# Optimization experiments

Hardware: AMD Instinct MI355X
Metric: run time of the kernel (lower is better)

The kernel has to match this reference:

```python
import jax, jax.numpy as jnp
import numpy as np

M_HIST = 5        # Anderson history depth (m=5 in anderson_solver)
N_POWER = 20      # power iterations to estimate sigma for spectral_norm
REG = 1e-4        # Tikhonov regularization on the Anderson LS system
MAX_ITER = 25     # deq_max_iter


def _l2norm(x):
    return x / (jnp.linalg.norm(x) + 1e-12)


def spectral_normalize(W):
    # torch spectral_norm: W / sigma, sigma = u^T W v with u,v from power iteration
    u = _l2norm(jnp.ones((W.shape[0],), W.dtype))
    def body(_, u):
        v = _l2norm(W.T @ u)
        return _l2norm(W @ v)
    u = jax.lax.fori_loop(0, N_POWER, body, u)
    v = _l2norm(W.T @ u)
    u = jax.lax.stop_gradient(u)
    v = jax.lax.stop_gradient(v)
    sigma = u @ (W @ v)
    return W / sigma


def make_f(W1, b1, W2, b2):
    W1s = spectral_normalize(W1)
    W2s = spectral_normalize(W2)
    def f(z, context):
        h = jnp.tanh(jnp.concatenate([z, context], axis=-1) @ W1s.T + b1)
        return jnp.tanh(h @ W2s.T + b2)
    return f


def anderson(f, x0, context, max_iter, m=M_HIST):
    # Mirrors anderson_solver, including its duplicated warm-up step.
    X = [x0]
    F = [f(x0, context)]
    x = F[0]; X.append(x); F.append(f(x, context))
    x = F[0]; X.append(x); F.append(f(x, context))
    for _k in range(2, max_iter):
        m_k = min(len(X) - 1, m)
        dX = jnp.stack([X[-i] - X[-i - 1] for i in range(1, m_k + 1)], axis=-1)  # [B,d,mk]
        dF = jnp.stack([F[-i] - F[-i - 1] for i in range(1, m_k + 1)], axis=-1)
        dG = dF - dX
        A = jnp.einsum('bdi,bdj->bij', dG, dG) + REG * jnp.eye(m_k, dtype=x0.dtype)
        r = F[-1] - X[-1]
        Bv = jnp.einsum('bdi,bd->bi', dG, r)
        alpha = jnp.linalg.solve(A, Bv[..., None])[..., 0]          # [B,mk]
        x = F[-1] - jnp.einsum('bdi,bi->bd', dF, alpha)
        X.append(x)
        F.append(f(x, context))
        if len(X) > m + 1:
            X.pop(0); F.pop(0)
    return X[-1]


def setup_inputs() -> dict:
    key = jax.random.key(0)
    ks = jax.random.split(key, 5)
    B, X_DIM, LATENT, HIDDEN = 2048, 256, 256, 1024
    context = jax.random.normal(ks[0], (B, X_DIM), jnp.float32)
    W1 = jax.random.normal(ks[1], (HIDDEN, LATENT + X_DIM), jnp.float32) / np.sqrt(LATENT + X_DIM)
    b1 = jax.random.normal(ks[2], (HIDDEN,), jnp.float32) * 0.01
    W2 = jax.random.normal(ks[3], (LATENT, HIDDEN), jnp.float32) / np.sqrt(HIDDEN)
    b2 = jax.random.normal(ks[4], (LATENT,), jnp.float32) * 0.01
    return {"context": context, "W1": W1, "b1": b1, "W2": W2, "b2": b2}


def reference(context, W1, b1, W2, b2):
    f = make_f(W1, b1, W2, b2)
    z0 = jnp.zeros((context.shape[0], W2.shape[0]), context.dtype)
    z_star = anderson(f, z0, context, MAX_ITER)
    return z_star
```

## Files before the change

### kernel.cpp

```cpp
#include <hip/hip_runtime.h>
#include <hip/hip_bf16.h>


#define B_ROWS 2048
#define D_LAT  256
#define D_CTX  256
#define D_HID  1024
#define KCAT   512
#define SLOT   (B_ROWS * D_LAT)
#define NRING  7

typedef __bf16 bf16x8 __attribute__((ext_vector_type(8)));
typedef float f32x4 __attribute__((ext_vector_type(4)));
typedef unsigned short u16;

__global__ void init_kernel(const float* __restrict__ ctx,
                            __hip_bfloat16* __restrict__ zc,
                            float* __restrict__ vA, float* __restrict__ uA,
                            float* __restrict__ G1p, float* __restrict__ G2) {
  int i = blockIdx.x * 256 + threadIdx.x;
  if (i < B_ROWS * KCAT) {
    int b = i >> 9, c = i & 511;
    float v = (c < 256) ? 0.0f : ctx[b * 256 + (c - 256)];
    zc[i] = __float2bfloat16(v);
  }
  if (i < 512 * 512) G1p[i] = 0.0f;
  if (i < 256 * 256) G2[i] = 0.0f;
  if (i < KCAT) vA[i] = 0.0f;
  if (i < D_LAT) uA[i] = 1.0f;
}

__global__ __launch_bounds__(256) void gram_kernel(
    const float* __restrict__ W1, const float* __restrict__ W2,
    float* __restrict__ G1p, float* __restrict__ G2) {
  __shared__ float As[32][66];
  __shared__ float Bs[32][34];
  const int tid = threadIdx.x;
  const int tx = tid & 15, ty = tid >> 4;

  const float* X; float* G; int N, ti, tj, k0base; bool modeA;
  int b = blockIdx.x;
  if (b < 1024) {
    modeA = true; X = W1; G = G1p; N = 512;
    int s = b >> 7, t = b & 127;
    ti = t >> 4; tj = t & 15; k0base = s * 128;
  } else {
    modeA = false; b -= 1024; X = W2; G = G2; N = 256;
    int s = b >> 5, t = b & 31;
    ti = t >> 3; tj = t & 7; k0base = s * 128;
  }

  float acc[4][2] = {};
  for (int k0 = k0base; k0 < k0base + 128; k0 += 32) {
    if (modeA) {
      for (int idx = tid; idx < 2048; idx += 256) {
        int r = idx & 63, c = idx >> 6;
        As[c][r] = X[(size_t)(k0 + c) * 512 + ti * 64 + r];
      }
      for (int idx = tid; idx < 1024; idx += 256) {
        int r = idx & 31, c = idx >> 5;
        Bs[c][r] = X[(size_t)(k0 + c) * 512 + tj * 32 + r];
      }
    } else {
      for (int idx = tid; idx < 2048; idx += 256) {
        int c = idx & 31, r = idx >> 5;
        As[c][r] = X[(size_t)(ti * 64 + r) * 1024 + k0 + c];
      }
      for (int idx = tid; idx < 1024; idx += 256) {
        int c = idx & 31, r = idx >> 5;
        Bs[c][r] = X[(size_t)(tj * 32 + r) * 1024 + k0 + c];
      }
    }
    __syncthreads();
#pragma unroll
    for (int kk = 0; kk < 32; kk++) {
      const float2* ap = (const float2*)&As[kk][ty * 4];
      float2 a0 = ap[0], a1 = ap[1];
      float2 b0 = *(const float2*)&Bs[kk][tx * 2];
      float a[4] = {a0.x, a0.y, a1.x, a1.y};
      float bb[2] = {b0.x, b0.y};
#pragma unroll
      for (int i = 0; i < 4; i++)
#pragma unroll
        for (int j = 0; j < 2; j++) acc[i][j] += a[i] * bb[j];
    }
    __syncthreads();
  }
#pragma unroll
  for (int i = 0; i < 4; i++)
#pragma unroll
    for (int j = 0; j < 2; j++)
      atomicAdd(&G[(size_t)(ti * 64 + ty * 4 + i) * N + tj * 32 + tx * 2 + j],
                acc[i][j]);
}

__global__ __launch_bounds__(256) void colsum_kernel(
    const float* __restrict__ W1, float* __restrict__ vA) {
  int b = blockIdx.x;
  for (int c = threadIdx.x; c < KCAT; c += 256) {
    float s = 0.f;
#pragma unroll
    for (int r = 0; r < 16; r++) s += W1[(size_t)(16 * b + r) * KCAT + c];
    atomicAdd(&vA[c], s);
  }
}

__global__ __launch_bounds__(256) void pmv_kernel(
    const float* __restrict__ G1p, const float* __restrict__ G2,
    const float* __restrict__ vi, float* __restrict__ vo,
    const float* __restrict__ ui, float* __restrict__ uo, int g1_active) {
  int gw = blockIdx.x * 4 + (threadIdx.x >> 6);
  int lane = threadIdx.x & 63;
  const float* G; const float* in; float* out; int n, r;
  if (gw < 512) {
    if (!g1_active) return;
    G = G1p; in = vi; out = vo; n = 512; r = gw;
  } else {
    G = G2; in = ui; out = uo; n = 256; r = gw - 512;
  }
  const float4* Gr = (const float4*)(G + (size_t)r * n);
  const float4* uv = (const float4*)in;
  float acc = 0.f;
  for (int c = lane; c < (n >> 2); c += 64) {
    float4 g = Gr[c], u = uv[c];
    acc += g.x * u.x + g.y * u.y + g.z * u.z + g.w * u.w;
  }
  for (int off = 32; off; off >>= 1) acc += __shfl_down(acc, off, 64);
  if (lane == 0) out[r] = 0.25f * acc;
}

__global__ __launch_bounds__(256) void sigma_kernel(
    const float* __restrict__ vA, const float* __restrict__ vB,
    const float* __restrict__ uA, const float* __restrict__ uB,
    float* __restrict__ sig) {
  float s[4] = {0.f, 0.f, 0.f, 0.f};
  for (int i = threadIdx.x; i < KCAT; i += 256) {
    s[0] += vA[i] * vB[i];
    s[1] += vA[i] * vA[i];
  }
  for (int i = threadIdx.x; i < D_LAT; i += 256) {
    s[2] += uA[i] * uA[i];
    s[3] += uA[i] * uB[i];
  }
  __shared__ float red[4][4];
  int lane = threadIdx.x & 63, w = threadIdx.x >> 6;
  for (int k = 0; k < 4; k++) {
    float a = s[k];
    for (int off = 32; off; off >>= 1) a += __shfl_down(a, off, 64);
    if (lane == 0) red[k][w] = a;
  }
  __syncthreads();
  if (threadIdx.x == 0) {
    float d0 = red[0][0] + red[0][1] + red[0][2] + red[0][3];
    float d1 = red[1][0] + red[1][1] + red[1][2] + red[1][3];
    float d2 = red[2][0] + red[2][1] + red[2][2] + red[2][3];
    float d3 = red[3][0] + red[3][1] + red[3][2] + red[3][3];
    sig[0] = sqrtf(0.25f * d0 / d1);
    sig[1] = sqrtf(0.25f * d2 / d3);
  }
}

__global__ void wfold_kernel(const float* __restrict__ W1,
                             const float* __restrict__ W2,
                             const float* __restrict__ sig,
                             __hip_bfloat16* __restrict__ W1b,
                             __hip_bfloat16* __restrict__ W2b) {
  int i = blockIdx.x * 256 + threadIdx.x;
  if (i < D_HID * KCAT) W1b[i] = __float2bfloat16(W1[i] * sig[0]);
  int j = i - D_HID * KCAT;
  if (j >= 0 && j < D_LAT * D_HID) W2b[j] = __float2bfloat16(W2[j] * sig[1]);
}

__global__ void warm1_kernel(const float* __restrict__ Fh,
                             float* __restrict__ Xh,
                             __hip_bfloat16* __restrict__ zc) {
  int i = blockIdx.x * 256 + threadIdx.x;
  float v = Fh[i];
  Xh[SLOT + i] = v;
  zc[(i >> 8) * KCAT + (i & 255)] = __float2bfloat16(v);
}
__global__ void warm2_kernel(const float* __restrict__ Fh,
                             float* __restrict__ Xh, float* __restrict__ Fw) {
  int i = blockIdx.x * 256 + threadIdx.x;
  Xh[2 * SLOT + i] = Fh[i];
  Fw[2 * SLOT + i] = Fh[SLOT + i];
}

template <int BM, int BN, bool OUT_BF16>
__global__ __launch_bounds__(256) void gemm_mfma(
    const __hip_bfloat16* __restrict__ A, const __hip_bfloat16* __restrict__ W,
    int K, const float* __restrict__ bias, float* __restrict__ Cf,
    __hip_bfloat16* __restrict__ Cb, int N) {
  __shared__ __align__(16) u16 lds[(BM + BN) * 64];
  u16* As = lds;
  u16* Ws = lds + BM * 64;
  const int tid = threadIdx.x;
  const int lane = tid & 63;
  const int wid = tid >> 6;
  const int wy = wid >> 1, wx = wid & 1;
  constexpr int WM = BM / 2, WN = BN / 2;
  constexpr int MB = WM / 16, NB = WN / 16;
  const int bm = blockIdx.x * BM;
  const int bn = blockIdx.y * BN;
  const int rlo = lane & 15, quad = lane >> 4;

  f32x4 acc[MB][NB] = {};

  for (int k0 = 0; k0 < K; k0 += 64) {
    for (int c = tid; c < BM * 8; c += 256) {
      int r = c >> 3, o = (c & 7) ^ (r & 7);
      __builtin_amdgcn_global_load_lds(
          (const __attribute__((address_space(1))) void*)(A + (size_t)(bm + r) * K + k0 + o * 8),
          (__attribute__((address_space(3))) void*)(As + c * 8), 16, 0, 0);
    }
    for (int c = tid; c < BN * 8; c += 256) {
      int r = c >> 3, o = (c & 7) ^ (r & 7);
      __builtin_amdgcn_global_load_lds(
          (const __attribute__((address_space(1))) void*)(W + (size_t)(bn + r) * K + k0 + o * 8),
          (__attribute__((address_space(3))) void*)(Ws + c * 8), 16, 0, 0);
    }
    __syncthreads();
#pragma unroll
    for (int kk = 0; kk < 2; kk++) {
      bf16x8 af[MB], bfr[NB];
#pragma unroll
      for (int mb = 0; mb < MB; mb++) {
        int r = wy * WM + mb * 16 + rlo;
        int o = (kk * 4 + quad) ^ (r & 7);
        af[mb] = *(const bf16x8*)(As + (r * 8 + o) * 8);
      }
#pragma unroll
      for (int nb = 0; nb < NB; nb++) {
        int r = wx * WN + nb * 16 + rlo;
        int o = (kk * 4 + quad) ^ (r & 7);
        bfr[nb] = *(const bf16x8*)(Ws + (r * 8 + o) * 8);
      }
#pragma unroll
      for (int mb = 0; mb < MB; mb++)
#pragma unroll
        for (int nb = 0; nb < NB; nb++)
          acc[mb][nb] = __builtin_amdgcn_mfma_f32_16x16x32_bf16(
              af[mb], bfr[nb], acc[mb][nb], 0, 0, 0);
    }
    __syncthreads();
  }

#pragma unroll
  for (int mb = 0; mb < MB; mb++) {
#pragma unroll
    for (int nb = 0; nb < NB; nb++) {
      int n = bn + wx * WN + nb * 16 + rlo;
      float bv = bias[n];
#pragma unroll
      for (int rg = 0; rg < 4; rg++) {
        int m = bm + wy * WM + mb * 16 + quad * 4 + rg;
        float val = tanhf(acc[mb][nb][rg] + bv);
        if constexpr (OUT_BF16) {
          Cb[(size_t)m * N + n] = __float2bfloat16(val);
        } else {
          Cf[(size_t)m * N + n] = val;
        }
      }
    }
  }
}

template <int MK>
__global__ __launch_bounds__(256) void anderson_step_kernel(
    const float* __restrict__ Xh, const float* __restrict__ Fh,
    float* __restrict__ Xw, __hip_bfloat16* __restrict__ zc, int t) {
  const int lane = threadIdx.x & 63;
  const int wid = threadIdx.x >> 6;
  const int b = blockIdx.x * 4 + wid;
  const int base = b * D_LAT + 4 * lane;

  f32x4 f[MK + 1], x[MK + 1];
#pragma unroll
  for (int i = 0; i <= MK; i++) {
    int sl = (t - 1 - i) % NRING;
    f[i] = *(const f32x4*)(Fh + (size_t)sl * SLOT + base);
    x[i] = *(const f32x4*)(Xh + (size_t)sl * SLOT + base);
  }

  const f32x4 r = f[0] - x[0];
  f32x4 dF[MK], dG[MK];
#pragma unroll
  for (int i = 0; i < MK; i++) {
    dF[i] = f[i] - f[i + 1];
    dG[i] = dF[i] - (x[i] - x[i + 1]);
  }

  constexpr int NV = MK * (MK + 1) / 2 + MK;
  float vals[NV];
  {
    int p = 0;
#pragma unroll
    for (int i = 0; i < MK; i++)
#pragma unroll
      for (int j = i; j < MK; j++) {
        f32x4 q = dG[i] * dG[j];
        vals[p++] = q[0] + q[1] + q[2] + q[3];
      }
#pragma unroll
    for (int i = 0; i < MK; i++) {
      f32x4 q = dG[i] * r;
      vals[p++] = q[0] + q[1] + q[2] + q[3];
    }
  }
#pragma unroll
  for (int off = 1; off <= 32; off <<= 1)
#pragma unroll
    for (int v = 0; v < NV; v++) vals[v] += __shfl_xor(vals[v], off, 64);

  float A[MK][MK], bv[MK], alpha[MK];
  {
    int p = 0;
#pragma unroll
    for (int i = 0; i < MK; i++)
#pragma unroll
      for (int j = i; j < MK; j++) {
        A[i][j] = vals[p];
        A[j][i] = vals[p];
        p++;
      }
#pragma unroll
    for (int i = 0; i < MK; i++) A[i][i] += 1e-4f;
#pragma unroll
    for (int i = 0; i < MK; i++) bv[i] = vals[p++];
  }

#pragma unroll
  for (int c = 0; c < MK; c++) {
    float inv = 1.0f / A[c][c];
#pragma unroll
    for (int rr = c + 1; rr < MK; rr++) {
      float fct = A[rr][c] * inv;
#pragma unroll
      for (int cc = c; cc < MK; cc++) A[rr][cc] -= fct * A[c][cc];
      bv[rr] -= fct * bv[c];
    }
  }
#pragma unroll
  for (int i = MK - 1; i >= 0; i--) {
    float s = bv[i];
#pragma unroll
    for (int j = i + 1; j < MK; j++) s -= A[i][j] * alpha[j];
    alpha[i] = s / A[i][i];
  }

  f32x4 xo = f[0];
#pragma unroll
  for (int i = 0; i < MK; i++) xo -= dF[i] * alpha[i];
  *(f32x4*)(Xw + base) = xo;
  if (zc != nullptr) {
    union { __hip_bfloat16 h[4]; unsigned long long u; } cv;
#pragma unroll
    for (int j = 0; j < 4; j++) cv.h[j] = __float2bfloat16(xo[j]);
    *(unsigned long long*)(zc + (size_t)b * KCAT + 4 * lane) = cv.u;
  }
}

static void eval_f(const __hip_bfloat16* zc, const __hip_bfloat16* W1b,
                   const __hip_bfloat16* W2b, const float* b1, const float* b2,
                   __hip_bfloat16* hb, float* Fout, hipStream_t stream) {
  gemm_mfma<64, 64, true><<<dim3(B_ROWS / 64, D_HID / 64), 256, 0, stream>>>(
      zc, W1b, KCAT, b1, nullptr, hb, D_HID);
  gemm_mfma<32, 32, false><<<dim3(B_ROWS / 32, D_LAT / 32), 256, 0, stream>>>(
      hb, W2b, D_HID, b2, Fout, nullptr, D_LAT);
}

extern "C" void kernel_launch(void* const* d_in, const int* in_sizes, int n_in,
                              void* d_out, int out_size, void* d_ws,
                              size_t ws_size, hipStream_t stream) {
  const float* ctx = (const float*)d_in[0];
  const float* W1 = (const float*)d_in[1];
  const float* b1 = (const float*)d_in[2];
  const float* W2 = (const float*)d_in[3];
  const float* b2 = (const float*)d_in[4];
  float* out = (float*)d_out;

  float* ws = (float*)d_ws;
  float* sig = ws;
  float* vA = ws + 16;
  float* vB = vA + KCAT;
  float* uA = vB + KCAT;
  float* uB = uA + D_LAT;
  float* G1p = uB + D_LAT;
  float* G2 = G1p + KCAT * KCAT;
  float* Xh = G2 + D_LAT * D_LAT;
  float* Fh = Xh + NRING * SLOT;
  __hip_bfloat16* W1b = (__hip_bfloat16*)(Fh + NRING * SLOT);
  __hip_bfloat16* W2b = W1b + D_HID * KCAT;
  __hip_bfloat16* zc = W2b + D_LAT * D_HID;
  __hip_bfloat16* hb = zc + B_ROWS * KCAT;

  init_kernel<<<(B_ROWS * KCAT + 255) / 256, 256, 0, stream>>>(ctx, zc, vA, uA,
                                                               G1p, G2);
  gram_kernel<<<1280, 256, 0, stream>>>(W1, W2, G1p, G2);
  colsum_kernel<<<64, 256, 0, stream>>>(W1, vA);

  for (int it = 1; it <= 21; it++) {
    const float* vi; float* vo;
    const float* ui; float* uo;
    if (it & 1) { vi = vB; vo = vA; ui = uA; uo = uB; }
    else        { vi = vA; vo = vB; ui = uB; uo = uA; }
    pmv_kernel<<<192, 256, 0, stream>>>(G1p, G2, vi, vo, ui, uo, it >= 2);
  }
  sigma_kernel<<<1, 256, 0, stream>>>(vA, vB, uA, uB, sig);
  wfold_kernel<<<(D_HID * KCAT + D_LAT * D_HID + 255) / 256, 256, 0, stream>>>(
      W1, W2, sig, W1b, W2b);

  hipMemsetAsync(Xh, 0, SLOT * sizeof(float), stream);

  eval_f(zc, W1b, W2b, b1, b2, hb, Fh, stream);
  warm1_kernel<<<SLOT / 256, 256, 0, stream>>>(Fh, Xh, zc);
  eval_f(zc, W1b, W2b, b1, b2, hb, Fh + SLOT, stream);
  warm2_kernel<<<SLOT / 256, 256, 0, stream>>>(Fh, Xh, Fh);

  for (int t = 3; t <= 25; t++) {
    int mk = (t - 1 < 5) ? (t - 1) : 5;
    float* Xw = (t == 25) ? out : (Xh + (t % NRING) * SLOT);
    __hip_bfloat16* zarg = (t == 25) ? nullptr : zc;
    dim3 g(B_ROWS / 4);
    if (mk == 2)
      anderson_step_kernel<2><<<g, 256, 0, stream>>>(Xh, Fh, Xw, zarg, t);
    else if (mk == 3)
      anderson_step_kernel<3><<<g, 256, 0, stream>>>(Xh, Fh, Xw, zarg, t);
    else if (mk == 4)
      anderson_step_kernel<4><<<g, 256, 0, stream>>>(Xh, Fh, Xw, zarg, t);
    else
      anderson_step_kernel<5><<<g, 256, 0, stream>>>(Xh, Fh, Xw, zarg, t);
    if (t < 25) {
      eval_f(zc, W1b, W2b, b1, b2, hb, Fh + (t % NRING) * SLOT, stream);
    }
  }
}
```

Measured before the change: 820.1 us.

## Double-buffer LDS in MFMA GEMM, template K, vectorize Gram loads

The bf16 MFMA GEMM now uses two LDS buffers. The next K-tile's global_load_lds runs while MFMAs compute the current tile, which removes one barrier per step. K becomes a template parameter so the loop can be fully unrolled and indexing can be folded at compile time. The fp32 Gram-matrix kernel used by spectral norm now loads float2 instead of scalars. LDS use doubles, which may reduce occupancy, and there is a single barrier between stage and compute, so correctness depends on the async load completing before that sync.

```diff
diff --git a/kernel.cpp b/kernel.cpp
--- a/kernel.cpp
+++ b/kernel.cpp
@@ -12,6 +12,7 @@
 
 typedef __bf16 bf16x8 __attribute__((ext_vector_type(8)));
 typedef float f32x4 __attribute__((ext_vector_type(4)));
+typedef float f32x2 __attribute__((ext_vector_type(2)));
 typedef unsigned short u16;
 
 __global__ void init_kernel(const float* __restrict__ ctx,
@@ -53,22 +54,28 @@
   float acc[4][2] = {};
   for (int k0 = k0base; k0 < k0base + 128; k0 += 32) {
     if (modeA) {
-      for (int idx = tid; idx < 2048; idx += 256) {
-        int r = idx & 63, c = idx >> 6;
-        As[c][r] = X[(size_t)(k0 + c) * 512 + ti * 64 + r];
-      }
       for (int idx = tid; idx < 1024; idx += 256) {
-        int r = idx & 31, c = idx >> 5;
-        Bs[c][r] = X[(size_t)(k0 + c) * 512 + tj * 32 + r];
+        int r2 = (idx & 31) * 2, c = idx >> 5;
+        f32x2 v = *(const f32x2*)(X + (size_t)(k0 + c) * 512 + ti * 64 + r2);
+        *(f32x2*)&As[c][r2] = v;
+      }
+      for (int idx = tid; idx < 512; idx += 256) {
+        int r2 = (idx & 15) * 2, c = idx >> 4;
+        f32x2 v = *(const f32x2*)(X + (size_t)(k0 + c) * 512 + tj * 32 + r2);
+        *(f32x2*)&Bs[c][r2] = v;
       }
     } else {
-      for (int idx = tid; idx < 2048; idx += 256) {
-        int c = idx & 31, r = idx >> 5;
-        As[c][r] = X[(size_t)(ti * 64 + r) * 1024 + k0 + c];
-      }
       for (int idx = tid; idx < 1024; idx += 256) {
-        int c = idx & 31, r = idx >> 5;
-        Bs[c][r] = X[(size_t)(tj * 32 + r) * 1024 + k0 + c];
+        int c2 = (idx & 15) * 2, r = idx >> 4;
+        f32x2 v = *(const f32x2*)(X + (size_t)(ti * 64 + r) * 1024 + k0 + c2);
+        As[c2][r] = v[0];
+        As[c2 + 1][r] = v[1];
+      }
+      for (int idx = tid; idx < 512; idx += 256) {
+        int c2 = (idx & 15) * 2, r = idx >> 4;
+        f32x2 v = *(const f32x2*)(X + (size_t)(tj * 32 + r) * 1024 + k0 + c2);
+        Bs[c2][r] = v[0];
+        Bs[c2 + 1][r] = v[1];
       }
     }
     __syncthreads();
@@ -186,27 +193,28 @@
   Fw[2 * SLOT + i] = Fh[SLOT + i];
 }
 
-template <int BM, int BN, bool OUT_BF16>
+template <int BM, int BN, int K, bool OUT_BF16>
 __global__ __launch_bounds__(256) void gemm_mfma(
     const __hip_bfloat16* __restrict__ A, const __hip_bfloat16* __restrict__ W,
-    int K, const float* __restrict__ bias, float* __restrict__ Cf,
+    const float* __restrict__ bias, float* __restrict__ Cf,
     __hip_bfloat16* __restrict__ Cb, int N) {
-  __shared__ __align__(16) u16 lds[(BM + BN) * 64];
-  u16* As = lds;
-  u16* Ws = lds + BM * 64;
+  __shared__ __align__(16) u16 lds[2][(BM + BN) * 64];
   const int tid = threadIdx.x;
   const int lane = tid & 63;
   const int wid = tid >> 6;
   const int wy = wid >> 1, wx = wid & 1;
   constexpr int WM = BM / 2, WN = BN / 2;
   constexpr int MB = WM / 16, NB = WN / 16;
+  constexpr int NK = K / 64;
   const int bm = blockIdx.x * BM;
   const int bn = blockIdx.y * BN;
   const int rlo = lane & 15, quad = lane >> 4;
 
   f32x4 acc[MB][NB] = {};
 
-  for (int k0 = 0; k0 < K; k0 += 64) {
+  auto stage = [&](u16* base, int k0) {
+    u16* As = base;
+    u16* Ws = base + BM * 64;
     for (int c = tid; c < BM * 8; c += 256) {
       int r = c >> 3, o = (c & 7) ^ (r & 7);
       __builtin_amdgcn_global_load_lds(
@@ -219,7 +227,10 @@
           (const __attribute__((address_space(1))) void*)(W + (size_t)(bn + r) * K + k0 + o * 8),
           (__attribute__((address_space(3))) void*)(Ws + c * 8), 16, 0, 0);
     }
-    __syncthreads();
+  };
+  auto compute = [&](const u16* base) {
+    const u16* As = base;
+    const u16* Ws = base + BM * 64;
 #pragma unroll
     for (int kk = 0; kk < 2; kk++) {
       bf16x8 af[MB], bfr[NB];
@@ -242,7 +253,17 @@
           acc[mb][nb] = __builtin_amdgcn_mfma_f32_16x16x32_bf16(
               af[mb], bfr[nb], acc[mb][nb], 0, 0, 0);
     }
-    __syncthreads();
+  };
+
+  stage(&lds[0][0], 0);
+  __syncthreads();
+#pragma unroll 2
+  for (int step = 0; step < NK; step++) {
+    u16* cur = (step & 1) ? &lds[1][0] : &lds[0][0];
+    u16* nxt = (step & 1) ? &lds[0][0] : &lds[1][0];
+    if (step + 1 < NK) stage(nxt, (step + 1) * 64);
+    compute(cur);
+    if (step + 1 < NK) __syncthreads();
   }
 
 #pragma unroll
@@ -363,10 +384,11 @@
 static void eval_f(const __hip_bfloat16* zc, const __hip_bfloat16* W1b,
                    const __hip_bfloat16* W2b, const float* b1, const float* b2,
                    __hip_bfloat16* hb, float* Fout, hipStream_t stream) {
-  gemm_mfma<64, 64, true><<<dim3(B_ROWS / 64, D_HID / 64), 256, 0, stream>>>(
-      zc, W1b, KCAT, b1, nullptr, hb, D_HID);
-  gemm_mfma<32, 32, false><<<dim3(B_ROWS / 32, D_LAT / 32), 256, 0, stream>>>(
-      hb, W2b, D_HID, b2, Fout, nullptr, D_LAT);
+  gemm_mfma<64, 64, KCAT, true><<<dim3(B_ROWS / 64, D_HID / 64), 256, 0,
+                                  stream>>>(zc, W1b, b1, nullptr, hb, D_HID);
+  gemm_mfma<32, 32, D_HID, false><<<dim3(B_ROWS / 32, D_LAT / 32), 256, 0,
+                                    stream>>>(hb, W2b, b2, Fout, nullptr,
+                                              D_LAT);
 }
 
 extern "C" void kernel_launch(void* const* d_in, const int* in_sizes, int n_in,
```

New measurement: 768.8 us. 6.3% less time.
